# Kernel optimization log

Measured on AMD Instinct MI355X. Metric: run time of the kernel, lower is better.

## Reference

```python
import jax, jax.numpy as jnp
import numpy as np

# Model config (matches init_kwargs)
DATA_L = 256
LATENT_L = 64
LATENT_N = 8
N_COMPS = 8
LOG_2PI = float(np.log(2.0 * np.pi))


def setup_inputs() -> dict:
    key = jax.random.key(0)
    ks = jax.random.split(key, 7)
    B = 2048
    N = B * LATENT_N  # 16384
    x = jax.random.normal(ks[0], (B, DATA_L), dtype=jnp.float32)
    W_e = jax.random.normal(ks[1], (DATA_L, LATENT_L * N_COMPS * 3), dtype=jnp.float32) * 0.05
    b_e = jnp.zeros((LATENT_L * N_COMPS * 3,), dtype=jnp.float32)
    W_d = jax.random.normal(ks[2], (LATENT_L, DATA_L * N_COMPS * 3), dtype=jnp.float32) * 0.05
    b_d = jnp.zeros((DATA_L * N_COMPS * 3,), dtype=jnp.float32)
    u_e = jax.random.normal(ks[3], (N, LATENT_L), dtype=jnp.float32)
    r = jax.random.uniform(ks[4], (N, LATENT_L), dtype=jnp.float32)
    return {"x": x, "W_e": W_e, "b_e": b_e, "W_d": W_d, "b_d": b_d, "u_e": u_e, "r": r}


def _split3(pred, K, D):
    # pred: (N, 3*K*D) -> m, logp, loga each (N, K, D)
    m = pred[:, : K * D].reshape(-1, K, D)
    logp = pred[:, K * D : 2 * K * D].reshape(-1, K, D)
    loga = pred[:, 2 * K * D :].reshape(-1, K, D)
    loga = jax.nn.log_softmax(loga, axis=1)  # loga - logsumexp over comps
    return m, logp, loga


def _discrete_sample(loga, r):
    # loga: (N, K, D), r: (N, D). Matches torch: idx = sum((r > cumsum(p)).int(), dim=1)
    c = jnp.cumsum(jnp.exp(loga), axis=1)  # (N, K, D)
    idx = jnp.sum((r[:, None, :] > c).astype(jnp.int32), axis=1)  # (N, D)
    return jnp.clip(idx, 0, loga.shape[1] - 1)


def reference(x, W_e, b_e, W_d, b_d, u_e, r):
    K, L, D = N_COMPS, LATENT_L, DATA_L
    x_rep = jnp.tile(x, (LATENT_N, 1))  # (N, D)

    # Encoder (KAN with width=[data_l, 3*K*L] modeled as dense layer)
    pred_e = x_rep @ W_e + b_e  # (N, 3*K*L)
    m_e, logp_e, loga_e = _split3(pred_e, K, L)

    # Sample mixture component per (row, latent dim), gather, reparameterize
    idx = _discrete_sample(loga_e, r)  # (N, L) int32
    m_sel = jnp.take_along_axis(m_e, idx[:, None, :], axis=1)[:, 0, :]  # (N, L)
    logp_sel = jnp.take_along_axis(logp_e, idx[:, None, :], axis=1)[:, 0, :]
    h = m_sel + jnp.exp(-0.5 * logp_sel) * u_e  # (N, L)

    # log q(h|x): mixture-of-Gaussians density at h
    uh = jnp.exp(0.5 * logp_e) * (h[:, None, :] - m_e)  # (N, K, L)
    L_e = jax.nn.logsumexp(loga_e - 0.5 * uh * uh + 0.5 * logp_e, axis=1)  # (N, L)
    L_e = -0.5 * L * LOG_2PI + jnp.sum(L_e, axis=1)  # (N,)

    # log prior N(0, I)
    L_q = -0.5 * L * LOG_2PI - 0.5 * jnp.sum(h * h, axis=1)  # (N,)

    # Decoder mixture likelihood of x
    pred_d = h @ W_d + b_d  # (N, 3*K*D)
    m_d, logp_d, loga_d = _split3(pred_d, K, D)
    ux = jnp.exp(0.5 * logp_d) * (x_rep[:, None, :] - m_d)  # (N, K, D)
    L_d = jax.nn.logsumexp(loga_d - 0.5 * ux * ux + 0.5 * logp_d, axis=1)  # (N, D)
    L_d = -0.5 * D * LOG_2PI + jnp.sum(L_d, axis=1)  # (N,)

    return -jnp.mean(L_d + L_q - L_e)
```

## Files before the change

kernel.cpp:

```cpp
#include <hip/hip_runtime.h>
#include <hip/hip_bf16.h>
#include <math.h>

#define D_L   256
#define L_L   64
#define K_C   8
#define BATCH 2048
#define NTOT  16384
#define ENC_COLS 1536
#define LOG2PI 1.8378770664093453f
#define L2E    1.4426950408889634f
#define LN2    0.6931471805599453f
#define C_HL2E 0.7213475204444817f

typedef __attribute__((ext_vector_type(8)))  short short8;
typedef __attribute__((ext_vector_type(8)))  unsigned short ushort8;
typedef __attribute__((ext_vector_type(4)))  unsigned short ushort4_;
typedef __attribute__((ext_vector_type(4)))  float float4_;
typedef __attribute__((ext_vector_type(16))) float float16_;

#if defined(__has_builtin)
#  if __has_builtin(__builtin_amdgcn_exp2f)
#    define EXP2F(x) __builtin_amdgcn_exp2f(x)
#  endif
#  if __has_builtin(__builtin_amdgcn_logf)
#    define LOG2F(x) __builtin_amdgcn_logf(x)
#  endif
#endif
#ifndef EXP2F
#  define EXP2F(x) __expf((x) * LN2)
#endif
#ifndef LOG2F
#  define LOG2F(x) (__logf(x) * L2E)
#endif

#define OFF_PE    0
#define OFF_H     (BATCH * ENC_COLS)
#define OFF_WET2  (OFF_H + NTOT * L_L / 2)
#define OFF_WDT2  (OFF_WET2 + ENC_COLS * D_L / 2)
#define OFF_ACC   (OFF_WDT2 + 6144 * 64 / 2)

__device__ __forceinline__ unsigned short f2bf(float f) {
  unsigned u = __float_as_uint(f);
  return (unsigned short)((u + 0x7fffu + ((u >> 16) & 1u)) >> 16);
}

__global__ __launch_bounds__(256) void k_prep(
    const float* __restrict__ We, const float* __restrict__ Wd,
    unsigned short* __restrict__ WeT2, unsigned short* __restrict__ WdT2,
    float* __restrict__ accf)
{
  const int bid = blockIdx.x, t = threadIdx.x;
  if (bid == 192) { if (t == 0) accf[0] = 0.0f; return; }

  const float* src; int C, rowbase, colbase; float scale;
  unsigned short* dst;
  if (bid < 96) {
    const int comp = bid / 12, p = (bid % 12) >> 2, dt = bid & 3;
    src = Wd; C = 6144; rowbase = 0;
    colbase = p * 2048 + comp * 256 + dt * 64;
    scale = p ? L2E : 1.0f;
    dst = WdT2 + (size_t)bid * 4096;
  } else {
    const int idx = bid - 96;
    src = We; C = ENC_COLS; rowbase = (idx & 3) * 64;
    colbase = (idx >> 2) * 64;
    scale = 1.0f;
    dst = WeT2 + (size_t)idx * 4096;
  }

  __shared__ float tile[64][65];
  {
    const int col = t & 63, w0 = t >> 6;
    #pragma unroll
    for (int i = 0; i < 16; ++i) {
      const int r = w0 + i * 4;
      tile[r][col] = src[(size_t)(rowbase + r) * C + colbase + col] * scale;
    }
  }
  __syncthreads();
  const int st = t >> 6, q = (t >> 5) & 1, c = t & 31;
  #pragma unroll
  for (int dg = 0; dg < 2; ++dg) {
    ushort8 o;
    #pragma unroll
    for (int j = 0; j < 8; ++j) o[j] = f2bf(tile[st * 16 + q * 8 + j][dg * 32 + c]);
    *(ushort8*)(dst + ((((size_t)dg * 4 + st) * 2 + q) * 32 + c) * 8) = o;
  }
}

__global__ __launch_bounds__(256) void k_enc(
    const float* __restrict__ x, const unsigned short* __restrict__ WeT2,
    const float* __restrict__ be, float* __restrict__ pe)
{
  __shared__ __align__(16) unsigned short as_[64 * 264];
  const int t = threadIdx.x;
  const int w = t >> 6, l = t & 63;
  const int col = l & 31, q = l >> 5;
  const int rg = w >> 1, dg = w & 1;
  const int m0 = blockIdx.y * 64, cblk = blockIdx.x, c0 = cblk * 64;

  {
    const int kc4 = (t & 63) * 4;
    #pragma unroll
    for (int i = 0; i < 16; ++i) {
      const int r = (t >> 6) + i * 4;
      float4_ v = *(const float4_*)(x + (size_t)(m0 + r) * D_L + kc4);
      ushort4_ o;
      o[0] = f2bf(v[0]); o[1] = f2bf(v[1]); o[2] = f2bf(v[2]); o[3] = f2bf(v[3]);
      *(ushort4_*)&as_[r * 264 + kc4] = o;
    }
  }

  const float bias = be[c0 + dg * 32 + col];
  float16_ acc;
  #pragma unroll
  for (int e = 0; e < 16; ++e) acc[e] = bias;

  __syncthreads();

  const unsigned short* arow = &as_[(rg * 32 + col) * 264 + q * 8];
  const unsigned short* bbase = WeT2 + (size_t)cblk * 16384 + dg * 2048 + l * 8;
  #pragma unroll
  for (int kc = 0; kc < 4; ++kc) {
    #pragma unroll
    for (int st = 0; st < 4; ++st) {
      short8 a = *(const short8*)(arow + kc * 64 + st * 16);
      short8 b = *(const short8*)(bbase + (size_t)kc * 4096 + st * 512);
      acc = __builtin_amdgcn_mfma_f32_32x32x16_bf16(a, b, acc, 0, 0, 0);
    }
  }
  #pragma unroll
  for (int e = 0; e < 16; ++e) {
    const int row = (e & 3) + 8 * (e >> 2) + 4 * q;
    pe[(size_t)(m0 + rg * 32 + row) * ENC_COLS + c0 + dg * 32 + col] = acc[e];
  }
}

__global__ __launch_bounds__(256) void k_enc_post(
    const float* __restrict__ pe, const float* __restrict__ ue,
    const float* __restrict__ rr, unsigned short* __restrict__ h,
    float* __restrict__ accf)
{
  const int lane = threadIdx.x & 63;
  const int w = threadIdx.x >> 6;
  const int b = blockIdx.x * 4 + w;
  const float* row = pe + (size_t)b * ENC_COLS + lane;

  float m[8], p[8], a[8];
  #pragma unroll
  for (int k = 0; k < K_C; ++k) {
    m[k] = row[k * 64]; p[k] = row[512 + k * 64]; a[k] = row[1024 + k * 64];
  }
  float amax = a[0];
  #pragma unroll
  for (int k = 1; k < K_C; ++k) amax = fmaxf(amax, a[k]);
  float sa = 0.f;
  #pragma unroll
  for (int k = 0; k < K_C; ++k) sa += __expf(a[k] - amax);
  const float lse_a = amax + __logf(sa);

  float cum[8];
  {
    float cs = 0.f;
    #pragma unroll
    for (int k = 0; k < K_C; ++k) { cs += __expf(a[k] - lse_a); cum[k] = cs; }
  }
  float ep[8];
  #pragma unroll
  for (int k = 0; k < K_C; ++k) ep[k] = __expf(p[k]);

  const int st = lane >> 4, qq = (lane >> 3) & 1, jj = lane & 7;

  float tot = 0.f;
  for (int j = 0; j < 8; ++j) {
    const int n = b + BATCH * j;
    const float rv = rr[(size_t)n * L_L + lane];
    const float uv = ue[(size_t)n * L_L + lane];
    int idx = 0;
    #pragma unroll
    for (int k = 0; k < K_C; ++k) idx += (rv > cum[k]) ? 1 : 0;
    idx = min(idx, K_C - 1);
    float msel = m[0], psel = p[0];
    #pragma unroll
    for (int k = 1; k < K_C; ++k) {
      const bool sel = (idx == k);
      msel = sel ? m[k] : msel;
      psel = sel ? p[k] : psel;
    }
    const float hv = fmaf(__expf(-0.5f * psel), uv, msel);

    const int nblk = n >> 6, rgn = (n >> 5) & 1, coln = n & 31;
    h[((((size_t)(nblk * 2 + rgn) * 4 + st) * 2 + qq) * 32 + coln) * 8 + jj] = f2bf(hv);

    float stt = 0.f;
    #pragma unroll
    for (int k = 0; k < K_C; ++k) {
      const float dd = hv - m[k];
      const float tt = a[k] + 0.5f * p[k] - 0.5f * ep[k] * dd * dd;
      stt += __expf(tt);
    }
    tot += -0.5f * hv * hv - (__logf(stt + 1e-30f) - lse_a);
  }
  #pragma unroll
  for (int off = 1; off < 64; off <<= 1) tot += __shfl_xor(tot, off, 64);
  __shared__ float red2[4];
  if (lane == 0) red2[w] = tot;
  __syncthreads();
  if (threadIdx.x == 0) atomicAdd(accf, red2[0] + red2[1] + red2[2] + red2[3]);
}

__global__ __launch_bounds__(256, 2) void k_dec(
    const unsigned short* __restrict__ hF, const float* __restrict__ x,
    const unsigned short* __restrict__ WdT2, const float* __restrict__ bd,
    float* __restrict__ accf)
{
  const int t = threadIdx.x;
  const int w = t >> 6, l = t & 63;
  const int col = l & 31, q = l >> 5;
  const int rg = w >> 1, dg = w & 1;
  const int dt = blockIdx.x, d0 = dt * 64;
  const int nblk = blockIdx.y, n0 = nblk * 64;
  const int colD = d0 + dg * 32 + col;

  const unsigned short* hbase = hF + ((size_t)(nblk * 2 + rg) * 4) * 512 + l * 8;
  short8 af[4];
  #pragma unroll
  for (int st = 0; st < 4; ++st) af[st] = *(const short8*)(hbase + st * 512);

  float xv[16];
  #pragma unroll
  for (int e = 0; e < 16; ++e) {
    const int rw = (e & 3) + 8 * (e >> 2) + 4 * q;
    const int n = n0 + rg * 32 + rw;
    xv[e] = x[(size_t)(n & (BATCH - 1)) * D_L + colD];
  }

  float s_a[16], s_t[16];
  #pragma unroll
  for (int e = 0; e < 16; ++e) { s_a[e] = 0.f; s_t[e] = 0.f; }

  const unsigned short* wbase = WdT2 + dg * 2048 + l * 8;

  for (int comp = 0; comp < K_C; ++comp) {
    const float bm  = bd[comp * 256 + colD];
    const float bpL = bd[2048 + comp * 256 + colD] * L2E;
    const float baL = bd[4096 + comp * 256 + colD] * L2E;

    short8 bf[3][4];
    #pragma unroll
    for (int p = 0; p < 3; ++p) {
      const unsigned short* pb = wbase + ((size_t)(comp * 3 + p) * 4 + dt) * 4096;
      #pragma unroll
      for (int st = 0; st < 4; ++st) bf[p][st] = *(const short8*)(pb + st * 512);
    }

    float16_ am = {}, ap = {}, aa = {};
    #pragma unroll
    for (int st = 0; st < 4; ++st) {
      am = __builtin_amdgcn_mfma_f32_32x32x16_bf16(af[st], bf[0][st], am, 0, 0, 0);
      ap = __builtin_amdgcn_mfma_f32_32x32x16_bf16(af[st], bf[1][st], ap, 0, 0, 0);
      aa = __builtin_amdgcn_mfma_f32_32x32x16_bf16(af[st], bf[2][st], aa, 0, 0, 0);
    }

    #pragma unroll
    for (int e = 0; e < 16; ++e) {
      const float dd  = xv[e] - (am[e] + bm);
      const float lpL = ap[e] + bpL;
      const float laL = aa[e] + baL;
      const float ex2 = EXP2F(lpL);
      const float t1  = fmaf(0.5f, lpL, laL);
      const float ttL = fmaf(-C_HL2E * ex2, dd * dd, t1);
      s_a[e] += EXP2F(laL);
      s_t[e] += EXP2F(ttL);
    }
  }

  float v = 0.f;
  #pragma unroll
  for (int e = 0; e < 16; ++e)
    v += LOG2F(s_t[e] + 1e-30f) - LOG2F(s_a[e]);
  v *= LN2;
  #pragma unroll
  for (int off = 1; off < 64; off <<= 1) v += __shfl_xor(v, off, 64);
  __shared__ float red[4];
  if (l == 0) red[w] = v;
  __syncthreads();
  if (t == 0) atomicAdd(accf, red[0] + red[1] + red[2] + red[3]);
}

__global__ void k_final(const float* __restrict__ accf, float* __restrict__ out)
{
  if (threadIdx.x == 0) out[0] = -(accf[0] / (float)NTOT) + 128.0f * LOG2PI;
}

extern "C" void kernel_launch(void* const* d_in, const int* in_sizes, int n_in,
                              void* d_out, int out_size, void* d_ws, size_t ws_size,
                              hipStream_t stream)
{
  const float* x  = (const float*)d_in[0];
  const float* We = (const float*)d_in[1];
  const float* be = (const float*)d_in[2];
  const float* Wd = (const float*)d_in[3];
  const float* bd = (const float*)d_in[4];
  const float* ue = (const float*)d_in[5];
  const float* rr = (const float*)d_in[6];
  float* out = (float*)d_out;

  float* ws = (float*)d_ws;
  float* pe            = ws + OFF_PE;
  unsigned short* h    = (unsigned short*)(ws + OFF_H);
  unsigned short* WeT2 = (unsigned short*)(ws + OFF_WET2);
  unsigned short* WdT2 = (unsigned short*)(ws + OFF_WDT2);
  float* accf          = ws + OFF_ACC;

  k_prep<<<dim3(193), 256, 0, stream>>>(We, Wd, WeT2, WdT2, accf);
  k_enc<<<dim3(ENC_COLS / 64, BATCH / 64), 256, 0, stream>>>(x, WeT2, be, pe);
  k_enc_post<<<dim3(BATCH / 4), 256, 0, stream>>>(pe, ue, rr, h, accf);
  k_dec<<<dim3(4, NTOT / 64), 256, 0, stream>>>(h, x, WdT2, bd, accf);
  k_final<<<dim3(1), 64, 0, stream>>>(accf, out);
}
```

Measured before the change: 123.8 us.

## Switch decoder to 16x16x32 MFMA tiles with relaid weights and fused final reduction

The decoder moves from 32x32x16 MFMA tiles over 64-row blocks to 16x16x32 MFMA tiles over 32-row blocks. Each wave now owns a 16-column slice, and the launch_bounds occupancy hint is removed. The prep and encoder-post kernels write the decoder weights and h in a new packed layout to match the new fragments. The separate final kernel is replaced by a last-block-done counter that writes the output, saving one launch at the cost of an extra atomic per block. Smaller tiles cut accumulator register pressure and add parallelism, but each MFMA does less work.

```diff
diff --git a/kernel.cpp b/kernel.cpp
--- a/kernel.cpp
+++ b/kernel.cpp
@@ -39,6 +39,7 @@
 #define OFF_WET2  (OFF_H + NTOT * L_L / 2)
 #define OFF_WDT2  (OFF_WET2 + ENC_COLS * D_L / 2)
 #define OFF_ACC   (OFF_WDT2 + 6144 * 64 / 2)
+#define OFF_CNT   (OFF_ACC + 1)
 
 __device__ __forceinline__ unsigned short f2bf(float f) {
   unsigned u = __float_as_uint(f);
@@ -48,44 +49,62 @@
 __global__ __launch_bounds__(256) void k_prep(
     const float* __restrict__ We, const float* __restrict__ Wd,
     unsigned short* __restrict__ WeT2, unsigned short* __restrict__ WdT2,
-    float* __restrict__ accf)
+    float* __restrict__ accf, unsigned* __restrict__ counter)
 {
   const int bid = blockIdx.x, t = threadIdx.x;
-  if (bid == 192) { if (t == 0) accf[0] = 0.0f; return; }
-
-  const float* src; int C, rowbase, colbase; float scale;
-  unsigned short* dst;
+  if (bid == 192) {
+    if (t == 0) { accf[0] = 0.0f; counter[0] = 0u; }
+    return;
+  }
+
+  __shared__ float tile[64][65];
+
   if (bid < 96) {
     const int comp = bid / 12, p = (bid % 12) >> 2, dt = bid & 3;
-    src = Wd; C = 6144; rowbase = 0;
-    colbase = p * 2048 + comp * 256 + dt * 64;
-    scale = p ? L2E : 1.0f;
-    dst = WdT2 + (size_t)bid * 4096;
+    const int colbase = p * 2048 + comp * 256 + dt * 64;
+    const float scale = p ? L2E : 1.0f;
+    {
+      const int col = t & 63, w0 = t >> 6;
+      #pragma unroll
+      for (int i = 0; i < 16; ++i) {
+        const int r = w0 + i * 4;
+        tile[r][col] = Wd[(size_t)r * 6144 + colbase + col] * scale;
+      }
+    }
+    __syncthreads();
+    const int lane = t & 63, q4 = lane >> 4, m_ = t & 15;
+    #pragma unroll
+    for (int ui = 0; ui < 2; ++ui) {
+      const int u = (t >> 6) + ui * 4;
+      const int db = u >> 1, kh = u & 1;
+      ushort8 o;
+      #pragma unroll
+      for (int j = 0; j < 8; ++j)
+        o[j] = f2bf(tile[kh * 32 + q4 * 8 + j][db * 16 + m_]);
+      *(ushort8*)(WdT2 +
+          ((((size_t)(comp * 3 + p) * 16 + dt * 4 + db) * 2 + kh) * 512) + lane * 8) = o;
+    }
   } else {
     const int idx = bid - 96;
-    src = We; C = ENC_COLS; rowbase = (idx & 3) * 64;
-    colbase = (idx >> 2) * 64;
-    scale = 1.0f;
-    dst = WeT2 + (size_t)idx * 4096;
-  }
-
-  __shared__ float tile[64][65];
-  {
-    const int col = t & 63, w0 = t >> 6;
-    #pragma unroll
-    for (int i = 0; i < 16; ++i) {
-      const int r = w0 + i * 4;
-      tile[r][col] = src[(size_t)(rowbase + r) * C + colbase + col] * scale;
-    }
-  }
-  __syncthreads();
-  const int st = t >> 6, q = (t >> 5) & 1, c = t & 31;
-  #pragma unroll
-  for (int dg = 0; dg < 2; ++dg) {
-    ushort8 o;
-    #pragma unroll
-    for (int j = 0; j < 8; ++j) o[j] = f2bf(tile[st * 16 + q * 8 + j][dg * 32 + c]);
-    *(ushort8*)(dst + ((((size_t)dg * 4 + st) * 2 + q) * 32 + c) * 8) = o;
+    const int rowbase = (idx & 3) * 64, colbase = (idx >> 2) * 64;
+    {
+      const int col = t & 63, w0 = t >> 6;
+      #pragma unroll
+      for (int i = 0; i < 16; ++i) {
+        const int r = w0 + i * 4;
+        tile[r][col] = We[(size_t)(rowbase + r) * ENC_COLS + colbase + col];
+      }
+    }
+    __syncthreads();
+    unsigned short* dst = WeT2 + (size_t)idx * 4096;
+    const int st = t >> 6, q = (t >> 5) & 1, c = t & 31;
+    #pragma unroll
+    for (int dg = 0; dg < 2; ++dg) {
+      ushort8 o;
+      #pragma unroll
+      for (int j = 0; j < 8; ++j) o[j] = f2bf(tile[st * 16 + q * 8 + j][dg * 32 + c]);
+      *(ushort8*)(dst + ((((size_t)dg * 4 + st) * 2 + q) * 32 + c) * 8) = o;
+    }
   }
 }
 
@@ -170,7 +189,7 @@
   #pragma unroll
   for (int k = 0; k < K_C; ++k) ep[k] = __expf(p[k]);
 
-  const int st = lane >> 4, qq = (lane >> 3) & 1, jj = lane & 7;
+  const int kh = lane >> 5, qd = (lane & 31) >> 3, jj = lane & 7;
 
   float tot = 0.f;
   for (int j = 0; j < 8; ++j) {
@@ -190,8 +209,8 @@
     }
     const float hv = fmaf(__expf(-0.5f * psel), uv, msel);
 
-    const int nblk = n >> 6, rgn = (n >> 5) & 1, coln = n & 31;
-    h[((((size_t)(nblk * 2 + rgn) * 4 + st) * 2 + qq) * 32 + coln) * 8 + jj] = f2bf(hv);
+    const int nb2 = n >> 5, rp = (n >> 4) & 1, mm = n & 15;
+    h[(((size_t)(nb2 * 2 + rp) * 2 + kh) * 512) + (qd * 16 + mm) * 8 + jj] = f2bf(hv);
 
     float stt = 0.f;
     #pragma unroll
@@ -210,75 +229,85 @@
   if (threadIdx.x == 0) atomicAdd(accf, red2[0] + red2[1] + red2[2] + red2[3]);
 }
 
-__global__ __launch_bounds__(256, 2) void k_dec(
+__global__ __launch_bounds__(256) void k_dec(
     const unsigned short* __restrict__ hF, const float* __restrict__ x,
     const unsigned short* __restrict__ WdT2, const float* __restrict__ bd,
-    float* __restrict__ accf)
+    float* __restrict__ accf, unsigned* __restrict__ counter,
+    float* __restrict__ out)
 {
   const int t = threadIdx.x;
   const int w = t >> 6, l = t & 63;
-  const int col = l & 31, q = l >> 5;
-  const int rg = w >> 1, dg = w & 1;
-  const int dt = blockIdx.x, d0 = dt * 64;
-  const int nblk = blockIdx.y, n0 = nblk * 64;
-  const int colD = d0 + dg * 32 + col;
-
-  const unsigned short* hbase = hF + ((size_t)(nblk * 2 + rg) * 4) * 512 + l * 8;
-  short8 af[4];
-  #pragma unroll
-  for (int st = 0; st < 4; ++st) af[st] = *(const short8*)(hbase + st * 512);
-
-  float xv[16];
-  #pragma unroll
-  for (int e = 0; e < 16; ++e) {
-    const int rw = (e & 3) + 8 * (e >> 2) + 4 * q;
-    const int n = n0 + rg * 32 + rw;
-    xv[e] = x[(size_t)(n & (BATCH - 1)) * D_L + colD];
-  }
-
-  float s_a[16], s_t[16];
-  #pragma unroll
-  for (int e = 0; e < 16; ++e) { s_a[e] = 0.f; s_t[e] = 0.f; }
-
-  const unsigned short* wbase = WdT2 + dg * 2048 + l * 8;
-
+  const int m = l & 15, quad = l >> 4;
+  const int by = blockIdx.y;
+  const int n0 = by * 32;
+  const int dblk = blockIdx.x * 4 + w;
+  const int dcol = dblk * 16 + m;
+
+  short8 af[2][2];
+  #pragma unroll
+  for (int rp = 0; rp < 2; ++rp)
+    #pragma unroll
+    for (int kh = 0; kh < 2; ++kh)
+      af[rp][kh] = *(const short8*)(hF +
+          (((size_t)(by * 2 + rp)) * 2 + kh) * 512 + l * 8);
+
+  float xv[8];
+  #pragma unroll
+  for (int rp = 0; rp < 2; ++rp)
+    #pragma unroll
+    for (int reg = 0; reg < 4; ++reg) {
+      const int n = n0 + rp * 16 + quad * 4 + reg;
+      xv[rp * 4 + reg] = x[(size_t)(n & (BATCH - 1)) * D_L + dcol];
+    }
+
+  float s_a[8], s_t[8];
+  #pragma unroll
+  for (int e = 0; e < 8; ++e) { s_a[e] = 0.f; s_t[e] = 0.f; }
+
+  const unsigned short* wbase = WdT2 + (size_t)dblk * 1024 + l * 8;
+
+  #pragma unroll 2
   for (int comp = 0; comp < K_C; ++comp) {
-    const float bm  = bd[comp * 256 + colD];
-    const float bpL = bd[2048 + comp * 256 + colD] * L2E;
-    const float baL = bd[4096 + comp * 256 + colD] * L2E;
-
-    short8 bf[3][4];
-    #pragma unroll
-    for (int p = 0; p < 3; ++p) {
-      const unsigned short* pb = wbase + ((size_t)(comp * 3 + p) * 4 + dt) * 4096;
-      #pragma unroll
-      for (int st = 0; st < 4; ++st) bf[p][st] = *(const short8*)(pb + st * 512);
-    }
-
-    float16_ am = {}, ap = {}, aa = {};
-    #pragma unroll
-    for (int st = 0; st < 4; ++st) {
-      am = __builtin_amdgcn_mfma_f32_32x32x16_bf16(af[st], bf[0][st], am, 0, 0, 0);
-      ap = __builtin_amdgcn_mfma_f32_32x32x16_bf16(af[st], bf[1][st], ap, 0, 0, 0);
-      aa = __builtin_amdgcn_mfma_f32_32x32x16_bf16(af[st], bf[2][st], aa, 0, 0, 0);
-    }
-
-    #pragma unroll
-    for (int e = 0; e < 16; ++e) {
-      const float dd  = xv[e] - (am[e] + bm);
-      const float lpL = ap[e] + bpL;
-      const float laL = aa[e] + baL;
-      const float ex2 = EXP2F(lpL);
-      const float t1  = fmaf(0.5f, lpL, laL);
-      const float ttL = fmaf(-C_HL2E * ex2, dd * dd, t1);
-      s_a[e] += EXP2F(laL);
-      s_t[e] += EXP2F(ttL);
+    const float bm  = bd[comp * 256 + dcol];
+    const float bpL = bd[2048 + comp * 256 + dcol] * L2E;
+    const float baL = bd[4096 + comp * 256 + dcol] * L2E;
+
+    short8 bf[3][2];
+    #pragma unroll
+    for (int p = 0; p < 3; ++p)
+      #pragma unroll
+      for (int kh = 0; kh < 2; ++kh)
+        bf[p][kh] = *(const short8*)(wbase +
+            ((size_t)(comp * 3 + p) * 16) * 1024 + kh * 512);
+
+    #pragma unroll
+    for (int rp = 0; rp < 2; ++rp) {
+      float4_ am = {}, ap = {}, aa = {};
+      am = __builtin_amdgcn_mfma_f32_16x16x32_bf16(af[rp][0], bf[0][0], am, 0, 0, 0);
+      ap = __builtin_amdgcn_mfma_f32_16x16x32_bf16(af[rp][0], bf[1][0], ap, 0, 0, 0);
+      aa = __builtin_amdgcn_mfma_f32_16x16x32_bf16(af[rp][0], bf[2][0], aa, 0, 0, 0);
+      am = __builtin_amdgcn_mfma_f32_16x16x32_bf16(af[rp][1], bf[0][1], am, 0, 0, 0);
+      ap = __builtin_amdgcn_mfma_f32_16x16x32_bf16(af[rp][1], bf[1][1], ap, 0, 0, 0);
+      aa = __builtin_amdgcn_mfma_f32_16x16x32_bf16(af[rp][1], bf[2][1], aa, 0, 0, 0);
+
+      #pragma unroll
+      for (int reg = 0; reg < 4; ++reg) {
+        const int e = rp * 4 + reg;
+        const float dd  = xv[e] - (am[reg] + bm);
+        const float lpL = ap[reg] + bpL;
+        const float laL = aa[reg] + baL;
+        const float ex2 = EXP2F(lpL);
+        const float t1  = fmaf(0.5f, lpL, laL);
+        const float ttL = fmaf(-C_HL2E * ex2, dd * dd, t1);
+        s_a[e] += EXP2F(laL);
+        s_t[e] += EXP2F(ttL);
+      }
     }
   }
 
   float v = 0.f;
   #pragma unroll
-  for (int e = 0; e < 16; ++e)
+  for (int e = 0; e < 8; ++e)
     v += LOG2F(s_t[e] + 1e-30f) - LOG2F(s_a[e]);
   v *= LN2;
   #pragma unroll
@@ -286,12 +315,17 @@
   __shared__ float red[4];
   if (l == 0) red[w] = v;
   __syncthreads();
-  if (t == 0) atomicAdd(accf, red[0] + red[1] + red[2] + red[3]);
-}
-
-__global__ void k_final(const float* __restrict__ accf, float* __restrict__ out)
-{
-  if (threadIdx.x == 0) out[0] = -(accf[0] / (float)NTOT) + 128.0f * LOG2PI;
+  if (t == 0) {
+    atomicAdd(accf, red[0] + red[1] + red[2] + red[3]);
+    __threadfence();
+    const unsigned c = atomicAdd(counter, 1u);
+    if (c == 2047u) {
+      __threadfence();
+      const float tot = __hip_atomic_load(accf, __ATOMIC_ACQUIRE,
+                                          __HIP_MEMORY_SCOPE_AGENT);
+      out[0] = -(tot / (float)NTOT) + 128.0f * LOG2PI;
+    }
+  }
 }
 
 extern "C" void kernel_launch(void* const* d_in, const int* in_sizes, int n_in,
@@ -313,10 +347,10 @@
   unsigned short* WeT2 = (unsigned short*)(ws + OFF_WET2);
   unsigned short* WdT2 = (unsigned short*)(ws + OFF_WDT2);
   float* accf          = ws + OFF_ACC;
-
-  k_prep<<<dim3(193), 256, 0, stream>>>(We, Wd, WeT2, WdT2, accf);
+  unsigned* counter    = (unsigned*)(ws + OFF_CNT);
+
+  k_prep<<<dim3(193), 256, 0, stream>>>(We, Wd, WeT2, WdT2, accf, counter);
   k_enc<<<dim3(ENC_COLS / 64, BATCH / 64), 256, 0, stream>>>(x, WeT2, be, pe);
   k_enc_post<<<dim3(BATCH / 4), 256, 0, stream>>>(pe, ue, rr, h, accf);
-  k_dec<<<dim3(4, NTOT / 64), 256, 0, stream>>>(h, x, WdT2, bd, accf);
-  k_final<<<dim3(1), 64, 0, stream>>>(accf, out);
-}
+  k_dec<<<dim3(4, NTOT / 32), 256, 0, stream>>>(h, x, WdT2, bd, accf, counter, out);
+}
```

Measured after the change: 165.4 us. +33.6%, slower.
